# Optimization experiments

Measured on AMD Instinct MI355X. Metric: run time of the kernel, lower is better.

## Reference

```python
import jax, jax.numpy as jnp
import numpy as np

N_NODES = 100000
N_EDGES = 3200000
IN_CH = 32
HID = 64


def gcn_conv(x, src, dst, W, b, n_nodes):
    """PyG GCNConv with default add_self_loops=True and symmetric normalization.
    out = D^{-1/2} (A + I) D^{-1/2} X W + b, where D is degree of A+I."""
    h = x @ W  # [N, out]
    ones = jnp.ones((src.shape[0],), dtype=h.dtype)
    deg = jax.ops.segment_sum(ones, dst, num_segments=n_nodes) + 1.0  # +1 self loop
    dinv = jax.lax.rsqrt(deg)  # [N]
    norm = dinv[src] * dinv[dst]  # [E]
    msgs = h[src] * norm[:, None]  # [E, out] gather (memory-bound)
    agg = jax.ops.segment_sum(msgs, dst, num_segments=n_nodes)  # scatter-add
    agg = agg + h * (1.0 / deg)[:, None]  # self-loop contribution (norm = 1/deg)
    return agg + b


def setup_inputs() -> dict:
    key = jax.random.key(0)
    ks = jax.random.split(key, 8)
    x = jax.random.normal(ks[0], (N_NODES, IN_CH), dtype=jnp.float32)
    edge_index = jax.random.randint(ks[1], (2, N_EDGES), 0, N_NODES, dtype=jnp.int64)
    # Glorot-style init for GCN weights, uniform for linear layer
    s1 = (6.0 / (IN_CH + HID)) ** 0.5
    s2 = (6.0 / (HID + HID)) ** 0.5
    W1 = jax.random.uniform(ks[2], (IN_CH, HID), jnp.float32, -s1, s1)
    b1 = jnp.zeros((HID,), jnp.float32)
    W2 = jax.random.uniform(ks[3], (HID, HID), jnp.float32, -s2, s2)
    b2 = jnp.zeros((HID,), jnp.float32)
    sc = 1.0 / (HID ** 0.5)
    Wc = jax.random.uniform(ks[4], (HID, 1), jnp.float32, -sc, sc)
    bc = jax.random.uniform(ks[5], (1,), jnp.float32, -sc, sc)
    return {"x": x, "edge_index": edge_index, "W1": W1, "b1": b1,
            "W2": W2, "b2": b2, "Wc": Wc, "bc": bc}


def reference(x, edge_index, W1, b1, W2, b2, Wc, bc):
    src, dst = edge_index[0], edge_index[1]
    n = x.shape[0]
    h = jax.nn.relu(gcn_conv(x, src, dst, W1, b1, n))
    h = jax.nn.relu(gcn_conv(h, src, dst, W2, b2, n))
    return jax.nn.sigmoid(h @ Wc + bc)  # [N, 1]
```

## Files before the change

### kernel.cpp

```cpp
#include <hip/hip_runtime.h>
#include <math.h>

#define N_NODES 100000
#define N_EDGES 3200000
#define IN_CH 32
#define HID 64
#define BW 512
#define NB ((N_NODES + BW - 1) / BW)
#define CAP 17408
#define K3_CHUNK 4096
#define K3_BLOCKS ((N_EDGES + K3_CHUNK - 1) / K3_CHUNK)

typedef unsigned short ushort_t;
typedef unsigned long long u64_t;

__device__ __forceinline__ float bflo(unsigned u) { return __uint_as_float(u << 16); }
__device__ __forceinline__ float bfhi(unsigned u) { return __uint_as_float(u & 0xffff0000u); }
__device__ __forceinline__ unsigned packbf(float a, float b) {
    unsigned ua = __float_as_uint(a); ua += 0x7fffu + ((ua >> 16) & 1u);
    unsigned ub = __float_as_uint(b); ub += 0x7fffu + ((ub >> 16) & 1u);
    return (ua >> 16) | (ub & 0xffff0000u);
}

__global__ void partition_kernel(const int* __restrict__ src, const int* __restrict__ dst,
                                 int* __restrict__ gcursor, int* __restrict__ gsw) {
    __shared__ int h[NB], lbase[NB], lcur[NB];
    int t = threadIdx.x;
    for (int i = t; i < NB; i += 256) { h[i] = 0; lcur[i] = 0; }
    __syncthreads();
    const int4* d4 = (const int4*)dst;
    const int4* s4 = (const int4*)src;
    int i0 = blockIdx.x * (K3_CHUNK / 4) + t;
#pragma unroll
    for (int j = 0; j < K3_CHUNK / 1024; ++j) {
        int i4 = i0 + j * 256;
        if (i4 < N_EDGES / 4) {
            int4 d = d4[i4];
            atomicAdd(&h[d.x >> 9], 1);
            atomicAdd(&h[d.y >> 9], 1);
            atomicAdd(&h[d.z >> 9], 1);
            atomicAdd(&h[d.w >> 9], 1);
        }
    }
    __syncthreads();
    for (int i = t; i < NB; i += 256)
        lbase[i] = h[i] ? atomicAdd(&gcursor[i], h[i]) : 0;
    __syncthreads();
#pragma unroll
    for (int j = 0; j < K3_CHUNK / 1024; ++j) {
        int i4 = i0 + j * 256;
        if (i4 < N_EDGES / 4) {
            int4 d = d4[i4];
            int4 s = s4[i4];
            int b, r, idx;
            b = d.x >> 9; r = atomicAdd(&lcur[b], 1); idx = lbase[b] + r;
            if (idx < CAP) gsw[(size_t)b * CAP + idx] = s.x | ((d.x & (BW - 1)) << 17);
            b = d.y >> 9; r = atomicAdd(&lcur[b], 1); idx = lbase[b] + r;
            if (idx < CAP) gsw[(size_t)b * CAP + idx] = s.y | ((d.y & (BW - 1)) << 17);
            b = d.z >> 9; r = atomicAdd(&lcur[b], 1); idx = lbase[b] + r;
            if (idx < CAP) gsw[(size_t)b * CAP + idx] = s.z | ((d.z & (BW - 1)) << 17);
            b = d.w >> 9; r = atomicAdd(&lcur[b], 1); idx = lbase[b] + r;
            if (idx < CAP) gsw[(size_t)b * CAP + idx] = s.w | ((d.w & (BW - 1)) << 17);
        }
    }
}

__global__ void scan_buckets_kernel(const int* __restrict__ gcursor, int* __restrict__ gbase,
                                    int* __restrict__ rowptr) {
    __shared__ int sa[256], sb[256];
    int t = threadIdx.x;
    int v = (t < NB) ? gcursor[t] : 0;
    sa[t] = v;
    __syncthreads();
    int* pa = sa; int* pb = sb;
    for (int off = 1; off < 256; off <<= 1) {
        int add = (t >= off) ? pa[t - off] : 0;
        pb[t] = pa[t] + add;
        __syncthreads();
        int* tmp = pa; pa = pb; pb = tmp;
    }
    int excl = pa[t] - v;
    if (t <= NB) gbase[t] = (t == NB) ? N_EDGES : excl;
    if (t == 0) rowptr[N_NODES] = N_EDGES;
}

__global__ __launch_bounds__(1024) void bucket_place_kernel(
        const int* __restrict__ gsw, const int* __restrict__ gcursor,
        const int* __restrict__ gbase, const float* __restrict__ X,
        int* __restrict__ rowptr, float* __restrict__ dinv, int* __restrict__ esw,
        ushort_t* __restrict__ Xs) {
    __shared__ int cnt[BW], exc[BW], cur[BW];
    __shared__ int sa[BW], sb[BW];
    int t = threadIdx.x;
    int k = blockIdx.x;
    int d0 = k * BW;
    if (t < BW) { cnt[t] = 0; cur[t] = 0; }
    __syncthreads();
    int total = gcursor[k];
    if (total > CAP) total = CAP;
    const int* reg = gsw + (size_t)k * CAP;
    for (int i = t; i < total; i += 1024)
        atomicAdd(&cnt[reg[i] >> 17], 1);
    __syncthreads();
    if (t < BW) sa[t] = cnt[t];
    __syncthreads();
    int* pa = sa; int* pb = sb;
    for (int off = 1; off < BW; off <<= 1) {
        if (t < BW) {
            int add = (t >= off) ? pa[t - off] : 0;
            pb[t] = pa[t] + add;
        }
        __syncthreads();
        int* tmp = pa; pa = pb; pb = tmp;
    }
    int cbase = gbase[k];
    if (t < BW) {
        int e_x = pa[t] - cnt[t];
        exc[t] = e_x;
        int d = d0 + t;
        if (d < N_NODES) {
            rowptr[d] = cbase + e_x;
            dinv[d] = rsqrtf((float)cnt[t] + 1.0f);
        }
    }
    __syncthreads();
    for (int i = t; i < total; i += 1024) {
        int u = reg[i];
        int ld = u >> 17;
        int r = atomicAdd(&cur[ld], 1);
        esw[cbase + exc[ld] + r] = u & 0x1FFFF;
    }
    const float4* X4 = (const float4*)X;
    for (int i = t; i < BW * 8; i += 1024) {
        int nl = i >> 3;
        int node = d0 + nl;
        if (node >= N_NODES) break;
        float di = rsqrtf((float)cnt[nl] + 1.0f);
        float4 v = X4[(size_t)node * 8 + (i & 7)];
        u64_t o = ((u64_t)packbf(v.z * di, v.w * di) << 32) | packbf(v.x * di, v.y * di);
        *(u64_t*)((uint2*)Xs + (size_t)node * 8 + (i & 7)) = o;
    }
}

__global__ void gather_x_kernel(const int* __restrict__ esw, const int* __restrict__ rowptr,
                                const float* __restrict__ dinv, const ushort_t* __restrict__ Xs,
                                ushort_t* __restrict__ y) {
    int t = threadIdx.x;
    int node = blockIdx.x * 4 + (t >> 6);
    int lane = t & 63;
    int g = lane >> 3, s = lane & 7;
    int beg = rowptr[node], end = rowptr[node + 1];
    const uint2* H8 = (const uint2*)Xs;
    float4 acc = make_float4(0.f, 0.f, 0.f, 0.f);
    int i = beg + g;
    for (; i + 8 < end; i += 16) {
        int s0 = esw[i];
        int s1 = esw[i + 8];
        uint2 v0 = H8[(size_t)s0 * 8 + s];
        uint2 v1 = H8[(size_t)s1 * 8 + s];
        acc.x += bflo(v0.x) + bflo(v1.x);
        acc.y += bfhi(v0.x) + bfhi(v1.x);
        acc.z += bflo(v0.y) + bflo(v1.y);
        acc.w += bfhi(v0.y) + bfhi(v1.y);
    }
    if (i < end) {
        int s0 = esw[i];
        uint2 v0 = H8[(size_t)s0 * 8 + s];
        acc.x += bflo(v0.x);
        acc.y += bfhi(v0.x);
        acc.z += bflo(v0.y);
        acc.w += bfhi(v0.y);
    }
    acc.x += __shfl_xor(acc.x, 8, 64);  acc.y += __shfl_xor(acc.y, 8, 64);
    acc.z += __shfl_xor(acc.z, 8, 64);  acc.w += __shfl_xor(acc.w, 8, 64);
    acc.x += __shfl_xor(acc.x, 16, 64); acc.y += __shfl_xor(acc.y, 16, 64);
    acc.z += __shfl_xor(acc.z, 16, 64); acc.w += __shfl_xor(acc.w, 16, 64);
    acc.x += __shfl_xor(acc.x, 32, 64); acc.y += __shfl_xor(acc.y, 32, 64);
    acc.z += __shfl_xor(acc.z, 32, 64); acc.w += __shfl_xor(acc.w, 32, 64);

    if (g == 0) {
        uint2 hn = H8[(size_t)node * 8 + s];
        float di = dinv[node];
        float rx = di * (acc.x + bflo(hn.x));
        float ry = di * (acc.y + bfhi(hn.x));
        float rz = di * (acc.z + bflo(hn.y));
        float rw = di * (acc.w + bfhi(hn.y));
        u64_t o = ((u64_t)packbf(rz, rw) << 32) | packbf(rx, ry);
        *(u64_t*)((uint2*)y + (size_t)node * 8 + s) = o;
    }
}

__global__ __launch_bounds__(256) void dense12_kernel(
        const ushort_t* __restrict__ ybf, const float* __restrict__ W1,
        const float* __restrict__ b1, const float* __restrict__ W2,
        const float* __restrict__ dinv, ushort_t* __restrict__ Hs2) {
    __shared__ float W1l[IN_CH * HID];
    __shared__ float W2l[HID * HID];
    __shared__ float Yl[32 * IN_CH];
    __shared__ float H1l[32 * HID];
    int t = threadIdx.x;
    int node0 = blockIdx.x * 32;
    for (int i = t; i < IN_CH * HID / 4; i += 256) ((float4*)W1l)[i] = ((const float4*)W1)[i];
    for (int i = t; i < HID * HID / 4; i += 256) ((float4*)W2l)[i] = ((const float4*)W2)[i];
    {
        uint2 v = ((const uint2*)ybf)[(size_t)node0 * 8 + t];
        int nl = t >> 3, ci = t & 7;
        Yl[nl * IN_CH + ci * 4 + 0] = bflo(v.x);
        Yl[nl * IN_CH + ci * 4 + 1] = bfhi(v.x);
        Yl[nl * IN_CH + ci * 4 + 2] = bflo(v.y);
        Yl[nl * IN_CH + ci * 4 + 3] = bfhi(v.y);
    }
    __syncthreads();
    int nl = t >> 3;
    int c8 = t & 7;
    int ch0 = c8 * 8;
    float4 bA = ((const float4*)b1)[c8 * 2];
    float4 bB = ((const float4*)b1)[c8 * 2 + 1];
    float a0 = bA.x, a1 = bA.y, a2 = bA.z, a3 = bA.w;
    float a4 = bB.x, a5 = bB.y, a6 = bB.z, a7 = bB.w;
#pragma unroll
    for (int k = 0; k < IN_CH; ++k) {
        float xv = Yl[nl * IN_CH + k];
        float4 wA = *(const float4*)&W1l[k * HID + ch0];
        float4 wB = *(const float4*)&W1l[k * HID + ch0 + 4];
        a0 += xv * wA.x; a1 += xv * wA.y; a2 += xv * wA.z; a3 += xv * wA.w;
        a4 += xv * wB.x; a5 += xv * wB.y; a6 += xv * wB.z; a7 += xv * wB.w;
    }
    float* hp = &H1l[nl * HID + ch0];
    hp[0] = fmaxf(a0, 0.f); hp[1] = fmaxf(a1, 0.f);
    hp[2] = fmaxf(a2, 0.f); hp[3] = fmaxf(a3, 0.f);
    hp[4] = fmaxf(a4, 0.f); hp[5] = fmaxf(a5, 0.f);
    hp[6] = fmaxf(a6, 0.f); hp[7] = fmaxf(a7, 0.f);
    __syncthreads();
    float r0 = 0.f, r1 = 0.f, r2 = 0.f, r3 = 0.f;
    float r4 = 0.f, r5 = 0.f, r6 = 0.f, r7 = 0.f;
#pragma unroll
    for (int k = 0; k < HID; ++k) {
        float hv = H1l[nl * HID + k];
        float4 wA = *(const float4*)&W2l[k * HID + ch0];
        float4 wB = *(const float4*)&W2l[k * HID + ch0 + 4];
        r0 += hv * wA.x; r1 += hv * wA.y; r2 += hv * wA.z; r3 += hv * wA.w;
        r4 += hv * wB.x; r5 += hv * wB.y; r6 += hv * wB.z; r7 += hv * wB.w;
    }
    int node = node0 + nl;
    float di = dinv[node];
    uint4 o;
    o.x = packbf(r0 * di, r1 * di);
    o.y = packbf(r2 * di, r3 * di);
    o.z = packbf(r4 * di, r5 * di);
    o.w = packbf(r6 * di, r7 * di);
    *(uint4*)(Hs2 + (size_t)node * HID + ch0) = o;
}

__global__ void gather_cls_kernel(const int* __restrict__ esw, const int* __restrict__ rowptr,
                                  const float* __restrict__ dinv, const ushort_t* __restrict__ Hs,
                                  const float* __restrict__ b,
                                  const float* __restrict__ Wc, const float* __restrict__ bc,
                                  float* __restrict__ out) {
    int t = threadIdx.x;
    int node = blockIdx.x * 4 + (t >> 6);
    int lane = t & 63;
    int g = lane >> 4, s = lane & 15;
    int beg = rowptr[node], end = rowptr[node + 1];
    int cnt = end - beg;
    const uint2* H8 = (const uint2*)Hs;
    float4 acc = make_float4(0.f, 0.f, 0.f, 0.f);
    int i = g;
    for (; i + 12 < cnt; i += 16) {
        int s0 = esw[beg + i];
        int s1 = esw[beg + i + 4];
        int s2 = esw[beg + i + 8];
        int s3 = esw[beg + i + 12];
        uint2 v0 = H8[(size_t)s0 * 16 + s];
        uint2 v1 = H8[(size_t)s1 * 16 + s];
        uint2 v2 = H8[(size_t)s2 * 16 + s];
        uint2 v3 = H8[(size_t)s3 * 16 + s];
        acc.x += (bflo(v0.x) + bflo(v1.x)) + (bflo(v2.x) + bflo(v3.x));
        acc.y += (bfhi(v0.x) + bfhi(v1.x)) + (bfhi(v2.x) + bfhi(v3.x));
        acc.z += (bflo(v0.y) + bflo(v1.y)) + (bflo(v2.y) + bflo(v3.y));
        acc.w += (bfhi(v0.y) + bfhi(v1.y)) + (bfhi(v2.y) + bfhi(v3.y));
    }
    for (; i < cnt; i += 4) {
        int s0 = esw[beg + i];
        uint2 v0 = H8[(size_t)s0 * 16 + s];
        acc.x += bflo(v0.x);
        acc.y += bfhi(v0.x);
        acc.z += bflo(v0.y);
        acc.w += bfhi(v0.y);
    }
    acc.x += __shfl_xor(acc.x, 16, 64); acc.y += __shfl_xor(acc.y, 16, 64);
    acc.z += __shfl_xor(acc.z, 16, 64); acc.w += __shfl_xor(acc.w, 16, 64);
    acc.x += __shfl_xor(acc.x, 32, 64); acc.y += __shfl_xor(acc.y, 32, 64);
    acc.z += __shfl_xor(acc.z, 32, 64); acc.w += __shfl_xor(acc.w, 32, 64);

    uint2 hn = H8[(size_t)node * 16 + s];
    float di = dinv[node];
    float4 bb = ((const float4*)b)[s];
    float rx = fmaxf(di * (acc.x + bflo(hn.x)) + bb.x, 0.f);
    float ry = fmaxf(di * (acc.y + bfhi(hn.x)) + bb.y, 0.f);
    float rz = fmaxf(di * (acc.z + bflo(hn.y)) + bb.z, 0.f);
    float rw = fmaxf(di * (acc.w + bfhi(hn.y)) + bb.w, 0.f);

    float4 wc = ((const float4*)Wc)[s];
    float v = rx * wc.x + ry * wc.y + rz * wc.z + rw * wc.w;
#pragma unroll
    for (int off = 1; off < 16; off <<= 1) v += __shfl_xor(v, off, 64);
    if (lane == 0) out[node] = 1.0f / (1.0f + expf(-(v + bc[0])));
}

extern "C" void kernel_launch(void* const* d_in, const int* in_sizes, int n_in,
                              void* d_out, int out_size, void* d_ws, size_t ws_size,
                              hipStream_t stream) {
    const float* x  = (const float*)d_in[0];
    const int* ei   = (const int*)d_in[1];
    const float* W1 = (const float*)d_in[2];
    const float* b1 = (const float*)d_in[3];
    const float* W2 = (const float*)d_in[4];
    const float* b2 = (const float*)d_in[5];
    const float* Wc = (const float*)d_in[6];
    const float* bc = (const float*)d_in[7];
    float* out = (float*)d_out;

    const int* src = ei;
    const int* dst = ei + N_EDGES;

    int*   gsw    = (int*)d_ws;
    int*   esw    = gsw + (size_t)NB * CAP;
    int*   rowptr = esw + N_EDGES;
    float* dinv   = (float*)(rowptr + N_NODES + 8);
    int*   gcursor= (int*)(dinv + N_NODES);
    int*   gbase  = gcursor + 512;
    ushort_t* Xs  = (ushort_t*)(gbase + 512);
    ushort_t* y   = Xs + (size_t)N_NODES * IN_CH;
    ushort_t* Hs2 = y + (size_t)N_NODES * IN_CH;

    int node32 = N_NODES / 32;
    int node4  = N_NODES / 4;

    hipMemsetAsync(gcursor, 0, NB * sizeof(int), stream);
    partition_kernel<<<K3_BLOCKS, 256, 0, stream>>>(src, dst, gcursor, gsw);
    scan_buckets_kernel<<<1, 256, 0, stream>>>(gcursor, gbase, rowptr);
    bucket_place_kernel<<<NB, 1024, 0, stream>>>(gsw, gcursor, gbase, x,
                                                 rowptr, dinv, esw, Xs);

    gather_x_kernel<<<node4, 256, 0, stream>>>(esw, rowptr, dinv, Xs, y);
    dense12_kernel<<<node32, 256, 0, stream>>>(y, W1, b1, W2, dinv, Hs2);

    gather_cls_kernel<<<node4, 256, 0, stream>>>(esw, rowptr, dinv, Hs2, b2, Wc, bc, out);
}
```

Baseline: 252.3 us.

## Fold bucket scan into placement, cache dst in LDS, widen gather loads

Removes the separate single-block scan kernel: each placement block now computes its own bucket base by summing the preceding bucket counts in shared memory. The partition kernel keeps the dst chunk in LDS so the second pass does not reread it from global memory. The first gather unrolls to four edges per iteration, and the classifier gather switches to 16-byte loads covering eight channels per lane with more edge groups. These cut launch count and global traffic and add memory-level parallelism, at the cost of more LDS, more registers and a redundant per-block reduction.

```diff
diff --git a/kernel.cpp b/kernel.cpp
--- a/kernel.cpp
+++ b/kernel.cpp
@@ -25,6 +25,7 @@
 __global__ void partition_kernel(const int* __restrict__ src, const int* __restrict__ dst,
                                  int* __restrict__ gcursor, int* __restrict__ gsw) {
     __shared__ int h[NB], lbase[NB], lcur[NB];
+    __shared__ int4 dcache[K3_CHUNK / 4];
     int t = threadIdx.x;
     for (int i = t; i < NB; i += 256) { h[i] = 0; lcur[i] = 0; }
     __syncthreads();
@@ -36,6 +37,7 @@
         int i4 = i0 + j * 256;
         if (i4 < N_EDGES / 4) {
             int4 d = d4[i4];
+            dcache[t + j * 256] = d;
             atomicAdd(&h[d.x >> 9], 1);
             atomicAdd(&h[d.y >> 9], 1);
             atomicAdd(&h[d.z >> 9], 1);
@@ -50,7 +52,7 @@
     for (int j = 0; j < K3_CHUNK / 1024; ++j) {
         int i4 = i0 + j * 256;
         if (i4 < N_EDGES / 4) {
-            int4 d = d4[i4];
+            int4 d = dcache[t + j * 256];
             int4 s = s4[i4];
             int b, r, idx;
             b = d.x >> 9; r = atomicAdd(&lcur[b], 1); idx = lbase[b] + r;
@@ -65,37 +67,25 @@
     }
 }
 
-__global__ void scan_buckets_kernel(const int* __restrict__ gcursor, int* __restrict__ gbase,
-                                    int* __restrict__ rowptr) {
-    __shared__ int sa[256], sb[256];
-    int t = threadIdx.x;
-    int v = (t < NB) ? gcursor[t] : 0;
-    sa[t] = v;
-    __syncthreads();
-    int* pa = sa; int* pb = sb;
-    for (int off = 1; off < 256; off <<= 1) {
-        int add = (t >= off) ? pa[t - off] : 0;
-        pb[t] = pa[t] + add;
-        __syncthreads();
-        int* tmp = pa; pa = pb; pb = tmp;
-    }
-    int excl = pa[t] - v;
-    if (t <= NB) gbase[t] = (t == NB) ? N_EDGES : excl;
-    if (t == 0) rowptr[N_NODES] = N_EDGES;
-}
-
 __global__ __launch_bounds__(1024) void bucket_place_kernel(
         const int* __restrict__ gsw, const int* __restrict__ gcursor,
-        const int* __restrict__ gbase, const float* __restrict__ X,
+        const float* __restrict__ X,
         int* __restrict__ rowptr, float* __restrict__ dinv, int* __restrict__ esw,
         ushort_t* __restrict__ Xs) {
     __shared__ int cnt[BW], exc[BW], cur[BW];
     __shared__ int sa[BW], sb[BW];
+    __shared__ int bsum[256];
     int t = threadIdx.x;
     int k = blockIdx.x;
     int d0 = k * BW;
     if (t < BW) { cnt[t] = 0; cur[t] = 0; }
-    __syncthreads();
+    if (t < 256) bsum[t] = (t < k && t < NB) ? gcursor[t] : 0;
+    __syncthreads();
+    for (int off = 128; off > 0; off >>= 1) {
+        if (t < off) bsum[t] += bsum[t + off];
+        __syncthreads();
+    }
+    int cbase = bsum[0];
     int total = gcursor[k];
     if (total > CAP) total = CAP;
     const int* reg = gsw + (size_t)k * CAP;
@@ -113,7 +103,6 @@
         __syncthreads();
         int* tmp = pa; pa = pb; pb = tmp;
     }
-    int cbase = gbase[k];
     if (t < BW) {
         int e_x = pa[t] - cnt[t];
         exc[t] = e_x;
@@ -123,6 +112,7 @@
             dinv[d] = rsqrtf((float)cnt[t] + 1.0f);
         }
     }
+    if (k == NB - 1 && t == 0) rowptr[N_NODES] = N_EDGES;
     __syncthreads();
     for (int i = t; i < total; i += 1024) {
         int u = reg[i];
@@ -153,19 +143,23 @@
     const uint2* H8 = (const uint2*)Xs;
     float4 acc = make_float4(0.f, 0.f, 0.f, 0.f);
     int i = beg + g;
-    for (; i + 8 < end; i += 16) {
-        int s0 = esw[i];
-        int s1 = esw[i + 8];
-        uint2 v0 = H8[(size_t)s0 * 8 + s];
-        uint2 v1 = H8[(size_t)s1 * 8 + s];
-        acc.x += bflo(v0.x) + bflo(v1.x);
-        acc.y += bfhi(v0.x) + bfhi(v1.x);
-        acc.z += bflo(v0.y) + bflo(v1.y);
-        acc.w += bfhi(v0.y) + bfhi(v1.y);
-    }
-    if (i < end) {
-        int s0 = esw[i];
-        uint2 v0 = H8[(size_t)s0 * 8 + s];
+    for (; i + 24 < end; i += 32) {
+        int e0 = esw[i];
+        int e1 = esw[i + 8];
+        int e2 = esw[i + 16];
+        int e3 = esw[i + 24];
+        uint2 v0 = H8[(size_t)e0 * 8 + s];
+        uint2 v1 = H8[(size_t)e1 * 8 + s];
+        uint2 v2 = H8[(size_t)e2 * 8 + s];
+        uint2 v3 = H8[(size_t)e3 * 8 + s];
+        acc.x += (bflo(v0.x) + bflo(v1.x)) + (bflo(v2.x) + bflo(v3.x));
+        acc.y += (bfhi(v0.x) + bfhi(v1.x)) + (bfhi(v2.x) + bfhi(v3.x));
+        acc.z += (bflo(v0.y) + bflo(v1.y)) + (bflo(v2.y) + bflo(v3.y));
+        acc.w += (bfhi(v0.y) + bfhi(v1.y)) + (bfhi(v2.y) + bfhi(v3.y));
+    }
+    for (; i < end; i += 8) {
+        int e0 = esw[i];
+        uint2 v0 = H8[(size_t)e0 * 8 + s];
         acc.x += bflo(v0.x);
         acc.y += bfhi(v0.x);
         acc.z += bflo(v0.y);
@@ -260,51 +254,59 @@
     int t = threadIdx.x;
     int node = blockIdx.x * 4 + (t >> 6);
     int lane = t & 63;
-    int g = lane >> 4, s = lane & 15;
+    int g = lane >> 3, s = lane & 7;
     int beg = rowptr[node], end = rowptr[node + 1];
     int cnt = end - beg;
-    const uint2* H8 = (const uint2*)Hs;
-    float4 acc = make_float4(0.f, 0.f, 0.f, 0.f);
+    const uint4* H16 = (const uint4*)Hs;
+    float a0 = 0.f, a1 = 0.f, a2 = 0.f, a3 = 0.f;
+    float a4 = 0.f, a5 = 0.f, a6 = 0.f, a7 = 0.f;
     int i = g;
-    for (; i + 12 < cnt; i += 16) {
-        int s0 = esw[beg + i];
-        int s1 = esw[beg + i + 4];
-        int s2 = esw[beg + i + 8];
-        int s3 = esw[beg + i + 12];
-        uint2 v0 = H8[(size_t)s0 * 16 + s];
-        uint2 v1 = H8[(size_t)s1 * 16 + s];
-        uint2 v2 = H8[(size_t)s2 * 16 + s];
-        uint2 v3 = H8[(size_t)s3 * 16 + s];
-        acc.x += (bflo(v0.x) + bflo(v1.x)) + (bflo(v2.x) + bflo(v3.x));
-        acc.y += (bfhi(v0.x) + bfhi(v1.x)) + (bfhi(v2.x) + bfhi(v3.x));
-        acc.z += (bflo(v0.y) + bflo(v1.y)) + (bflo(v2.y) + bflo(v3.y));
-        acc.w += (bfhi(v0.y) + bfhi(v1.y)) + (bfhi(v2.y) + bfhi(v3.y));
-    }
-    for (; i < cnt; i += 4) {
-        int s0 = esw[beg + i];
-        uint2 v0 = H8[(size_t)s0 * 16 + s];
-        acc.x += bflo(v0.x);
-        acc.y += bfhi(v0.x);
-        acc.z += bflo(v0.y);
-        acc.w += bfhi(v0.y);
-    }
-    acc.x += __shfl_xor(acc.x, 16, 64); acc.y += __shfl_xor(acc.y, 16, 64);
-    acc.z += __shfl_xor(acc.z, 16, 64); acc.w += __shfl_xor(acc.w, 16, 64);
-    acc.x += __shfl_xor(acc.x, 32, 64); acc.y += __shfl_xor(acc.y, 32, 64);
-    acc.z += __shfl_xor(acc.z, 32, 64); acc.w += __shfl_xor(acc.w, 32, 64);
-
-    uint2 hn = H8[(size_t)node * 16 + s];
+    for (; i + 8 < cnt; i += 16) {
+        int e0 = esw[beg + i];
+        int e1 = esw[beg + i + 8];
+        uint4 v0 = H16[(size_t)e0 * 8 + s];
+        uint4 v1 = H16[(size_t)e1 * 8 + s];
+        a0 += bflo(v0.x) + bflo(v1.x); a1 += bfhi(v0.x) + bfhi(v1.x);
+        a2 += bflo(v0.y) + bflo(v1.y); a3 += bfhi(v0.y) + bfhi(v1.y);
+        a4 += bflo(v0.z) + bflo(v1.z); a5 += bfhi(v0.z) + bfhi(v1.z);
+        a6 += bflo(v0.w) + bflo(v1.w); a7 += bfhi(v0.w) + bfhi(v1.w);
+    }
+    if (i < cnt) {
+        int e0 = esw[beg + i];
+        uint4 v0 = H16[(size_t)e0 * 8 + s];
+        a0 += bflo(v0.x); a1 += bfhi(v0.x);
+        a2 += bflo(v0.y); a3 += bfhi(v0.y);
+        a4 += bflo(v0.z); a5 += bfhi(v0.z);
+        a6 += bflo(v0.w); a7 += bfhi(v0.w);
+    }
+#define RED8(m) \
+    a0 += __shfl_xor(a0, m, 64); a1 += __shfl_xor(a1, m, 64); \
+    a2 += __shfl_xor(a2, m, 64); a3 += __shfl_xor(a3, m, 64); \
+    a4 += __shfl_xor(a4, m, 64); a5 += __shfl_xor(a5, m, 64); \
+    a6 += __shfl_xor(a6, m, 64); a7 += __shfl_xor(a7, m, 64);
+    RED8(8) RED8(16) RED8(32)
+#undef RED8
+
+    uint4 hn = H16[(size_t)node * 8 + s];
     float di = dinv[node];
-    float4 bb = ((const float4*)b)[s];
-    float rx = fmaxf(di * (acc.x + bflo(hn.x)) + bb.x, 0.f);
-    float ry = fmaxf(di * (acc.y + bfhi(hn.x)) + bb.y, 0.f);
-    float rz = fmaxf(di * (acc.z + bflo(hn.y)) + bb.z, 0.f);
-    float rw = fmaxf(di * (acc.w + bfhi(hn.y)) + bb.w, 0.f);
-
-    float4 wc = ((const float4*)Wc)[s];
-    float v = rx * wc.x + ry * wc.y + rz * wc.z + rw * wc.w;
-#pragma unroll
-    for (int off = 1; off < 16; off <<= 1) v += __shfl_xor(v, off, 64);
+    float4 bA = ((const float4*)b)[s * 2];
+    float4 bB = ((const float4*)b)[s * 2 + 1];
+    float r0 = fmaxf(di * (a0 + bflo(hn.x)) + bA.x, 0.f);
+    float r1 = fmaxf(di * (a1 + bfhi(hn.x)) + bA.y, 0.f);
+    float r2 = fmaxf(di * (a2 + bflo(hn.y)) + bA.z, 0.f);
+    float r3 = fmaxf(di * (a3 + bfhi(hn.y)) + bA.w, 0.f);
+    float r4 = fmaxf(di * (a4 + bflo(hn.z)) + bB.x, 0.f);
+    float r5 = fmaxf(di * (a5 + bfhi(hn.z)) + bB.y, 0.f);
+    float r6 = fmaxf(di * (a6 + bflo(hn.w)) + bB.z, 0.f);
+    float r7 = fmaxf(di * (a7 + bfhi(hn.w)) + bB.w, 0.f);
+
+    float4 wA = ((const float4*)Wc)[s * 2];
+    float4 wB = ((const float4*)Wc)[s * 2 + 1];
+    float v = r0 * wA.x + r1 * wA.y + r2 * wA.z + r3 * wA.w
+            + r4 * wB.x + r5 * wB.y + r6 * wB.z + r7 * wB.w;
+    v += __shfl_xor(v, 1, 64);
+    v += __shfl_xor(v, 2, 64);
+    v += __shfl_xor(v, 4, 64);
     if (lane == 0) out[node] = 1.0f / (1.0f + expf(-(v + bc[0])));
 }
 
@@ -329,8 +331,7 @@
     int*   rowptr = esw + N_EDGES;
     float* dinv   = (float*)(rowptr + N_NODES + 8);
     int*   gcursor= (int*)(dinv + N_NODES);
-    int*   gbase  = gcursor + 512;
-    ushort_t* Xs  = (ushort_t*)(gbase + 512);
+    ushort_t* Xs  = (ushort_t*)(gcursor + 512);
     ushort_t* y   = Xs + (size_t)N_NODES * IN_CH;
     ushort_t* Hs2 = y + (size_t)N_NODES * IN_CH;
 
@@ -339,8 +340,7 @@
 
     hipMemsetAsync(gcursor, 0, NB * sizeof(int), stream);
     partition_kernel<<<K3_BLOCKS, 256, 0, stream>>>(src, dst, gcursor, gsw);
-    scan_buckets_kernel<<<1, 256, 0, stream>>>(gcursor, gbase, rowptr);
-    bucket_place_kernel<<<NB, 1024, 0, stream>>>(gsw, gcursor, gbase, x,
+    bucket_place_kernel<<<NB, 1024, 0, stream>>>(gsw, gcursor, x,
                                                  rowptr, dinv, esw, Xs);
 
     gather_x_kernel<<<node4, 256, 0, stream>>>(esw, rowptr, dinv, Xs, y);
```

Result: no change. 251.6 us (-0.3%).
